# Kernel tuning notes

Hardware: AMD Instinct MI355X
Metric: run time of the kernel (lower is better)

Reference implementation:

```python
import jax, jax.numpy as jnp
import numpy as np

N_HEAD = 16
N_KV_HEAD = 4
N_EMBD = 2048

def rotate_half(x):
    x1, x2 = jnp.split(x, 2, axis=-1)
    return jnp.concatenate([-x2, x1], axis=-1)

def rope_tables(T, k):
    # angles = 10000^(-2*i/k) for i in [0, k/2); cos/sin repeated twice along last dim
    inv = jnp.power(10000.0, -2.0 * jnp.arange(k // 2, dtype=jnp.float32) / k)
    ang = jnp.arange(T, dtype=jnp.float32)[:, None] * inv[None, :]  # [T, k/2]
    cos = jnp.tile(jnp.cos(ang), (1, 2))  # [T, k]
    sin = jnp.tile(jnp.sin(ang), (1, 2))
    return cos, sin

def setup_inputs() -> dict:
    key = jax.random.key(0)
    ks = jax.random.split(key, 5)
    B, T, D = 4, 1024, N_EMBD
    g, h = N_KV_HEAD, N_HEAD
    k = D // h
    s = 0.02
    return {
        'x': jax.random.normal(ks[0], (B, T, D), dtype=jnp.float32),
        'Wq': jax.random.normal(ks[1], (D, D), dtype=jnp.float32) * s,
        'Wk': jax.random.normal(ks[2], (D, g * k), dtype=jnp.float32) * s,
        'Wv': jax.random.normal(ks[3], (D, g * k), dtype=jnp.float32) * s,
        'Wo': jax.random.normal(ks[4], (D, D), dtype=jnp.float32) * s,
    }

def reference(x, Wq, Wk, Wv, Wo):
    B, T, D = x.shape
    h, g = N_HEAD, N_KV_HEAD
    k = D // h
    Q = (x @ Wq).reshape(B, T, h, k).transpose(0, 2, 1, 3)  # [B,h,T,k]
    K = (x @ Wk).reshape(B, T, g, k).transpose(0, 2, 1, 3)  # [B,g,T,k]
    V = (x @ Wv).reshape(B, T, g, k).transpose(0, 2, 1, 3)
    # GQA: repeat_interleave kv heads to match query heads
    K = jnp.repeat(K, h // g, axis=1)  # [B,h,T,k]
    V = jnp.repeat(V, h // g, axis=1)
    cos, sin = rope_tables(T, k)
    cos = cos[None, None]  # [1,1,T,k]
    sin = sin[None, None]
    Q = Q * cos + rotate_half(Q) * sin
    K = K * cos + rotate_half(K) * sin
    scores = jnp.einsum('bhqk,bhsk->bhqs', Q, K) / jnp.sqrt(jnp.float32(k))
    causal = jnp.tril(jnp.ones((T, T), dtype=bool))
    scores = jnp.where(causal[None, None], scores, -jnp.inf)
    A = jax.nn.softmax(scores, axis=-1)
    Y = jnp.einsum('bhqs,bhsk->bhqk', A, V)
    Y = Y.transpose(0, 2, 1, 3).reshape(B, T, D)
    return Y @ Wo
```

## Files before the change

### kernel.cpp

```cpp
#include <hip/hip_runtime.h>
#include <math.h>

#define B_ 4
#define T_ 1024
#define D_ 2048
#define NH 16
#define NKV 4
#define HD 128
#define KV_D 512
#define QKV_S 2560

typedef __attribute__((ext_vector_type(8))) short short8;
typedef __attribute__((ext_vector_type(4))) float f32x4;

__device__ __forceinline__ ushort f2b(float f) {
    unsigned u = __float_as_uint(f);
    return (ushort)((u + 0x7fffu + ((u >> 16) & 1u)) >> 16);
}
__device__ __forceinline__ float b2f(ushort u) {
    return __uint_as_float((unsigned)u << 16);
}

#if __has_builtin(__builtin_amdgcn_exp2f)
#define EXP2F(x) __builtin_amdgcn_exp2f(x)
#else
#define EXP2F(x) __expf((x) * 0.6931471805599453f)
#endif

#define ASYNC_COPY16(g, l)                                                  \
    __builtin_amdgcn_global_load_lds(                                       \
        (const __attribute__((address_space(1))) void*)(g),                 \
        (__attribute__((address_space(3))) void*)(l), 16, 0, 0)

__global__ __launch_bounds__(256) void prep_all(const float* __restrict__ x,
                                                const float* __restrict__ Wq,
                                                const float* __restrict__ Wk,
                                                const float* __restrict__ Wv,
                                                const float* __restrict__ Wo,
                                                ushort* __restrict__ xb,
                                                ushort* __restrict__ WqkvT,
                                                ushort* __restrict__ WoT,
                                                float2* __restrict__ tab) {
    __shared__ float tile[32][33];
    const int bid = blockIdx.x;
    if (bid < 8192) {
        const int i = bid * 256 + threadIdx.x;
        const float4 v = ((const float4*)x)[i];
        ushort4 u;
        u.x = f2b(v.x); u.y = f2b(v.y); u.z = f2b(v.z); u.w = f2b(v.w);
        ((ushort4*)xb)[i] = u;
        return;
    }
    if (bid >= 18432) {
        const int idx = (bid - 18432) * 256 + threadIdx.x;
        const int t = idx >> 6, i = idx & 63;
        const float inv = exp2f((float)i * (-13.287712379549449f / 64.0f));
        const float ang = (float)t * inv;
        tab[idx] = make_float2(cosf(ang), sinf(ang));
        return;
    }
    const float* W;
    ushort* WT;
    int N, rb;
    if (bid < 12288)      { W = Wq; WT = WqkvT;                           N = D_;   rb = bid - 8192; }
    else if (bid < 13312) { W = Wk; WT = WqkvT + (size_t)D_ * D_;         N = KV_D; rb = bid - 12288; }
    else if (bid < 14336) { W = Wv; WT = WqkvT + (size_t)(D_+KV_D) * D_;  N = KV_D; rb = bid - 13312; }
    else                  { W = Wo; WT = WoT;                             N = D_;   rb = bid - 14336; }
    const int bxn = N / 32;
    const int n0 = (rb % bxn) * 32, k0 = (rb / bxn) * 32;
    const int tx = threadIdx.x & 31, ty = threadIdx.x >> 5;
    for (int i = ty; i < 32; i += 8)
        tile[i][tx] = W[(size_t)(k0 + i) * N + n0 + tx];
    __syncthreads();
    for (int i = ty; i < 32; i += 8)
        WT[(size_t)(n0 + i) * D_ + k0 + tx] = f2b(tile[tx][i]);
}

__global__ __launch_bounds__(256) void gemm_qkv(const ushort* __restrict__ A,
                                                const ushort* __restrict__ BT,
                                                ushort* __restrict__ QKV,
                                                ushort* __restrict__ Vt,
                                                const float2* __restrict__ tab) {
    __shared__ ushort smem[128 * 136];
    ushort* As = smem;
    ushort* Bs = smem + 4096;
    const int K = D_;
    const int tid = threadIdx.x;
    const int m0 = blockIdx.y * 128, n0 = blockIdx.x * 128;
    const int hid = n0 >> 7;
    const int wave = tid >> 6, lane = tid & 63;
    const int wm = (wave >> 1) * 64, wn = (wave & 1) * 64;
    const int lrow = lane & 15;
    const int quad = lane >> 4;

    f32x4 acc[4][4];
    const f32x4 zero = {0.f, 0.f, 0.f, 0.f};
#pragma unroll
    for (int i = 0; i < 4; ++i)
#pragma unroll
        for (int j = 0; j < 4; ++j) acc[i][j] = zero;

    const int srow = tid >> 2;
    const int scol = (tid & 3) * 8;
    const ushort* Ag = A + (size_t)(m0 + srow) * K + scol;
    const ushort* Bg = BT + (size_t)(n0 + srow) * K + scol;
    ushort* AsT = As + tid * 8;
    ushort* BsT = Bs + tid * 8;

    for (int k0 = 0; k0 < K; k0 += 32) {
        ASYNC_COPY16(Ag + k0, AsT);
        ASYNC_COPY16(Ag + k0 + (size_t)64 * K, AsT + 64 * 32);
        ASYNC_COPY16(Bg + k0, BsT);
        ASYNC_COPY16(Bg + k0 + (size_t)64 * K, BsT + 64 * 32);
        __syncthreads();

        short8 a[4], b[4];
#pragma unroll
        for (int mt = 0; mt < 4; ++mt)
            a[mt] = *(const short8*)&As[(wm + mt * 16 + lrow) * 32 + quad * 8];
#pragma unroll
        for (int nt = 0; nt < 4; ++nt)
            b[nt] = *(const short8*)&Bs[(wn + nt * 16 + lrow) * 32 + quad * 8];
#pragma unroll
        for (int mt = 0; mt < 4; ++mt)
#pragma unroll
            for (int nt = 0; nt < 4; ++nt)
                acc[mt][nt] = __builtin_amdgcn_mfma_f32_16x16x32_bf16(
                    a[mt], b[nt], acc[mt][nt], 0, 0, 0);
        __syncthreads();
    }

    ushort* Epi = smem;
#pragma unroll
    for (int mt = 0; mt < 4; ++mt)
#pragma unroll
        for (int nt = 0; nt < 4; ++nt)
#pragma unroll
            for (int r = 0; r < 4; ++r)
                Epi[(wm + mt * 16 + quad * 4 + r) * 136 + wn + nt * 16 + lrow] =
                    f2b(acc[mt][nt][r]);
    __syncthreads();

    const int b = m0 >> 10;
    const int t0 = m0 & 1023;

    if (hid < NH + NKV) {
        const bool isQ = hid < NH;
        const size_t colbase = isQ ? hid * HD : (size_t)D_ + (hid - NH) * HD;
        const float sc = isQ ? (0.08838834764831845f * 1.4426950408889634f) : 1.0f;
        const int r = tid >> 1;
        const int hf = tid & 1;
        const int t = t0 + r;
        ushort* orow = QKV + (size_t)(m0 + r) * QKV_S + colbase;
        const float4* tab4 = (const float4*)tab;
#pragma unroll
        for (int jj = 0; jj < 4; ++jj) {
            const int dbase = hf * 32 + jj * 8;
            const short8 lo = *(const short8*)&Epi[r * 136 + dbase];
            const short8 hi = *(const short8*)&Epi[r * 136 + 64 + dbase];
            ushort olo[8], ohi[8];
#pragma unroll
            for (int k = 0; k < 4; ++k) {
                const float4 cs = tab4[((t * 64 + dbase) >> 1) + k];
                const float x1a = b2f(lo[2 * k]),     x2a = b2f(hi[2 * k]);
                const float x1b = b2f(lo[2 * k + 1]), x2b = b2f(hi[2 * k + 1]);
                olo[2 * k]     = f2b((x1a * cs.x - x2a * cs.y) * sc);
                ohi[2 * k]     = f2b((x2a * cs.x + x1a * cs.y) * sc);
                olo[2 * k + 1] = f2b((x1b * cs.z - x2b * cs.w) * sc);
                ohi[2 * k + 1] = f2b((x2b * cs.z + x1b * cs.w) * sc);
            }
            *(short8*)&orow[dbase]      = *(short8*)olo;
            *(short8*)&orow[dbase + 64] = *(short8*)ohi;
        }
    } else {
        const int kv = hid - (NH + NKV);
        const int d = tid & 127;
        const int hf = tid >> 7;
        ushort* vrow = Vt + ((size_t)((b * NKV + kv) * HD + d)) * T_ + t0 + hf * 64;
#pragma unroll
        for (int jj = 0; jj < 8; ++jj) {
            ushort pk[8];
#pragma unroll
            for (int k = 0; k < 8; ++k)
                pk[k] = Epi[(hf * 64 + jj * 8 + k) * 136 + d];
            *(short8*)&vrow[jj * 8] = *(short8*)pk;
        }
    }
}

__global__ __launch_bounds__(256) void gemm_bf16(const ushort* __restrict__ A,
                                                 const ushort* __restrict__ BT,
                                                 float* __restrict__ C,
                                                 int M, int N, int K) {
    __shared__ ushort As[128 * 32];
    __shared__ ushort Bs[128 * 32];
    const int tid = threadIdx.x;
    const int m0 = blockIdx.y * 128, n0 = blockIdx.x * 128;
    const int wave = tid >> 6, lane = tid & 63;
    const int wm = (wave >> 1) * 64, wn = (wave & 1) * 64;
    const int lrow = lane & 15;
    const int quad = lane >> 4;

    f32x4 acc[4][4];
    const f32x4 zero = {0.f, 0.f, 0.f, 0.f};
#pragma unroll
    for (int i = 0; i < 4; ++i)
#pragma unroll
        for (int j = 0; j < 4; ++j) acc[i][j] = zero;

    const int srow = tid >> 2;
    const int scol = (tid & 3) * 8;
    const ushort* Ag = A + (size_t)(m0 + srow) * K + scol;
    const ushort* Bg = BT + (size_t)(n0 + srow) * K + scol;
    ushort* AsT = As + tid * 8;
    ushort* BsT = Bs + tid * 8;

    for (int k0 = 0; k0 < K; k0 += 32) {
        ASYNC_COPY16(Ag + k0, AsT);
        ASYNC_COPY16(Ag + k0 + (size_t)64 * K, AsT + 64 * 32);
        ASYNC_COPY16(Bg + k0, BsT);
        ASYNC_COPY16(Bg + k0 + (size_t)64 * K, BsT + 64 * 32);
        __syncthreads();

        short8 a[4], b[4];
#pragma unroll
        for (int mt = 0; mt < 4; ++mt)
            a[mt] = *(const short8*)&As[(wm + mt * 16 + lrow) * 32 + quad * 8];
#pragma unroll
        for (int nt = 0; nt < 4; ++nt)
            b[nt] = *(const short8*)&Bs[(wn + nt * 16 + lrow) * 32 + quad * 8];
#pragma unroll
        for (int mt = 0; mt < 4; ++mt)
#pragma unroll
            for (int nt = 0; nt < 4; ++nt)
                acc[mt][nt] = __builtin_amdgcn_mfma_f32_16x16x32_bf16(
                    a[mt], b[nt], acc[mt][nt], 0, 0, 0);
        __syncthreads();
    }

    const int crow = quad * 4;
    const int ccol = lrow;
#pragma unroll
    for (int mt = 0; mt < 4; ++mt)
#pragma unroll
        for (int nt = 0; nt < 4; ++nt)
#pragma unroll
            for (int r = 0; r < 4; ++r)
                C[(size_t)(m0 + wm + mt * 16 + crow + r) * N +
                  n0 + wn + nt * 16 + ccol] = acc[mt][nt][r];
}

__global__ __launch_bounds__(256) void attn_mfma(const ushort* __restrict__ QKV,
                                                 const ushort* __restrict__ Vt,
                                                 ushort* __restrict__ Yb) {
    __shared__ ushort Ks[64][136];
    __shared__ ushort Vs[128][72];
    __shared__ ushort Ps[4][16][72];

    const int bh = blockIdx.x;
    const int qt = (int)gridDim.y - 1 - (int)blockIdx.y;
    const int b = bh >> 4, h = bh & 15;
    const int kvh = h >> 2;
    const int q0 = qt * 64;
    const int tid = threadIdx.x;
    const int wave = tid >> 6, lane = tid & 63;
    const int ln = lane & 15, quad = lane >> 4;

    short8 qf[4];
    {
        const ushort* qp = QKV + ((size_t)(b * T_ + q0 + wave * 16 + ln)) * QKV_S + h * HD + quad * 8;
#pragma unroll
        for (int f = 0; f < 4; ++f) qf[f] = *(const short8*)(qp + f * 32);
    }

    f32x4 acc[8];
    const f32x4 zero = {0.f, 0.f, 0.f, 0.f};
#pragma unroll
    for (int j = 0; j < 8; ++j) acc[j] = zero;
    float m_r[4], l_r[4];
#pragma unroll
    for (int r = 0; r < 4; ++r) { m_r[r] = -INFINITY; l_r[r] = 0.f; }

    const int qrow = q0 + wave * 16 + quad * 4;

    for (int kt = 0; kt <= qt; ++kt) {
        const int s0 = kt * 64;
        __syncthreads();
#pragma unroll
        for (int c = 0; c < 4; ++c) {
            const int cid = tid + 256 * c;
            const int s = cid >> 4, ch = cid & 15;
            *(short8*)&Ks[s][ch * 8] =
                *(const short8*)&QKV[((size_t)(b * T_ + s0 + s)) * QKV_S + D_ + kvh * HD + ch * 8];
        }
#pragma unroll
        for (int c = 0; c < 4; ++c) {
            const int cid = tid + 256 * c;
            const int d = cid >> 3, ch = cid & 7;
            *(short8*)&Vs[d][ch * 8] =
                *(const short8*)&Vt[((size_t)((b * NKV + kvh) * HD + d)) * T_ + s0 + ch * 8];
        }
        __syncthreads();

        float sc[4][4];
#pragma unroll
        for (int ct = 0; ct < 4; ++ct) {
            f32x4 s4 = zero;
#pragma unroll
            for (int f = 0; f < 4; ++f)
                s4 = __builtin_amdgcn_mfma_f32_16x16x32_bf16(
                    qf[f], *(const short8*)&Ks[ct * 16 + ln][f * 32 + quad * 8], s4, 0, 0, 0);
#pragma unroll
            for (int r = 0; r < 4; ++r) sc[ct][r] = s4[r];
        }
        if (kt == qt) {
#pragma unroll
            for (int ct = 0; ct < 4; ++ct)
#pragma unroll
                for (int r = 0; r < 4; ++r)
                    if (s0 + ct * 16 + ln > qrow + r) sc[ct][r] = -INFINITY;
        }
        float alpha[4];
#pragma unroll
        for (int r = 0; r < 4; ++r) {
            float mx = fmaxf(fmaxf(sc[0][r], sc[1][r]), fmaxf(sc[2][r], sc[3][r]));
            mx = fmaxf(mx, __shfl_xor(mx, 1));
            mx = fmaxf(mx, __shfl_xor(mx, 2));
            mx = fmaxf(mx, __shfl_xor(mx, 4));
            mx = fmaxf(mx, __shfl_xor(mx, 8));
            const float mnew = fmaxf(m_r[r], mx);
            alpha[r] = EXP2F(m_r[r] - mnew);
            m_r[r] = mnew;
#pragma unroll
            for (int ct = 0; ct < 4; ++ct) sc[ct][r] = EXP2F(sc[ct][r] - mnew);
            float sum = (sc[0][r] + sc[1][r]) + (sc[2][r] + sc[3][r]);
            sum += __shfl_xor(sum, 1);
            sum += __shfl_xor(sum, 2);
            sum += __shfl_xor(sum, 4);
            sum += __shfl_xor(sum, 8);
            l_r[r] = l_r[r] * alpha[r] + sum;
        }
#pragma unroll
        for (int ct = 0; ct < 4; ++ct)
#pragma unroll
            for (int r = 0; r < 4; ++r)
                Ps[wave][quad * 4 + r][ct * 16 + ln] = f2b(sc[ct][r]);
#pragma unroll
        for (int j = 0; j < 8; ++j)
#pragma unroll
            for (int r = 0; r < 4; ++r) acc[j][r] *= alpha[r];
        const short8 pa0 = *(const short8*)&Ps[wave][ln][quad * 8];
        const short8 pa1 = *(const short8*)&Ps[wave][ln][32 + quad * 8];
#pragma unroll
        for (int j = 0; j < 8; ++j) {
            acc[j] = __builtin_amdgcn_mfma_f32_16x16x32_bf16(
                pa0, *(const short8*)&Vs[j * 16 + ln][quad * 8], acc[j], 0, 0, 0);
            acc[j] = __builtin_amdgcn_mfma_f32_16x16x32_bf16(
                pa1, *(const short8*)&Vs[j * 16 + ln][32 + quad * 8], acc[j], 0, 0, 0);
        }
    }

    float invl[4];
#pragma unroll
    for (int r = 0; r < 4; ++r) invl[r] = 1.f / l_r[r];
    ushort* yb = Yb + ((size_t)(b * T_ + qrow)) * D_ + h * HD + ln;
#pragma unroll
    for (int r = 0; r < 4; ++r)
#pragma unroll
        for (int j = 0; j < 8; ++j)
            yb[(size_t)r * D_ + j * 16] = f2b(acc[j][r] * invl[r]);
}

extern "C" void kernel_launch(void* const* d_in, const int* in_sizes, int n_in,
                              void* d_out, int out_size, void* d_ws, size_t ws_size,
                              hipStream_t stream) {
    const float* x  = (const float*)d_in[0];
    const float* Wq = (const float*)d_in[1];
    const float* Wk = (const float*)d_in[2];
    const float* Wv = (const float*)d_in[3];
    const float* Wo = (const float*)d_in[4];
    float* out = (float*)d_out;

    char* w = (char*)d_ws;
    ushort* xb    = (ushort*)w;  w += (size_t)4096 * D_ * 2;
    ushort* WqkvT = (ushort*)w;  w += (size_t)3072 * D_ * 2;
    ushort* QKV   = (ushort*)w;  w += (size_t)4096 * QKV_S * 2;
    ushort* Vt    = (ushort*)w;  w += (size_t)B_ * KV_D * T_ * 2;
    ushort* Yb    = (ushort*)w;  w += (size_t)4096 * D_ * 2;
    ushort* WoT   = (ushort*)w;  w += (size_t)D_ * D_ * 2;
    float2* tab   = (float2*)w;  w += (size_t)T_ * 64 * 8;

    const int M = B_ * T_;
    dim3 blk(256);

    prep_all<<<18688, blk, 0, stream>>>(x, Wq, Wk, Wv, Wo, xb, WqkvT, WoT, tab);

    gemm_qkv<<<dim3(3072 / 128, M / 128), blk, 0, stream>>>(xb, WqkvT, QKV, Vt, tab);

    attn_mfma<<<dim3(B_ * NH, T_ / 64), blk, 0, stream>>>(QKV, Vt, Yb);

    gemm_bf16<<<dim3(D_ / 128, M / 128), blk, 0, stream>>>(Yb, WoT, out, M, D_, D_);
}
```

Before: 298.3 us.

## Replace QKV GEMM with 256x256 double-buffered, swizzled, phase-scheduled MFMA kernel

The fused QKV projection GEMM moves from 128x128 tiles with 256 threads to 256x256 tiles with 512 threads. It uses 128 KB of dynamic LDS, double-buffers the K=64 slices, and XOR-swizzles the LDS layout. The main loop is split into four MFMA phases with explicit barriers, waitcnts, sched_barriers and setprio, so global-to-LDS copies for the next slice overlap with math. The RoPE/V-transpose epilogue is done in two 128-column halves. The larger tile raises data reuse and hides load latency, but the grid drops to 192 blocks, which may leave some CUs idle.

```diff
diff --git a/kernel.cpp b/kernel.cpp
--- a/kernel.cpp
+++ b/kernel.cpp
@@ -31,6 +31,22 @@
     __builtin_amdgcn_global_load_lds(                                       \
         (const __attribute__((address_space(1))) void*)(g),                 \
         (__attribute__((address_space(3))) void*)(l), 16, 0, 0)
+
+#define SBAR()                                                              \
+    do {                                                                    \
+        __builtin_amdgcn_sched_barrier(0);                                  \
+        asm volatile("" ::: "memory");                                      \
+        __builtin_amdgcn_s_barrier();                                       \
+        asm volatile("" ::: "memory");                                      \
+        __builtin_amdgcn_sched_barrier(0);                                  \
+    } while (0)
+#define WAITV(n) asm volatile("s_waitcnt vmcnt(" #n ")" ::: "memory")
+#define LGKM0()                                                             \
+    do {                                                                    \
+        asm volatile("s_waitcnt lgkmcnt(0)" ::: "memory");                  \
+        __builtin_amdgcn_sched_barrier(0);                                  \
+    } while (0)
+#define MFMA16(ap, bp, cc) cc = __builtin_amdgcn_mfma_f32_16x16x32_bf16(ap, bp, cc, 0, 0, 0)
 
 __global__ __launch_bounds__(256) void prep_all(const float* __restrict__ x,
                                                 const float* __restrict__ Wq,
@@ -76,115 +92,219 @@
         WT[(size_t)(n0 + i) * D_ + k0 + tx] = f2b(tile[tx][i]);
 }
 
-__global__ __launch_bounds__(256) void gemm_qkv(const ushort* __restrict__ A,
-                                                const ushort* __restrict__ BT,
-                                                ushort* __restrict__ QKV,
-                                                ushort* __restrict__ Vt,
-                                                const float2* __restrict__ tab) {
-    __shared__ ushort smem[128 * 136];
-    ushort* As = smem;
-    ushort* Bs = smem + 4096;
+__global__ __launch_bounds__(512, 2) void gemm_qkv256(const ushort* __restrict__ A,
+                                                      const ushort* __restrict__ BT,
+                                                      ushort* __restrict__ QKV,
+                                                      ushort* __restrict__ Vt,
+                                                      const float2* __restrict__ tab) {
+    extern __shared__ ushort smem[];
     const int K = D_;
+    const int NT = K / 64;
     const int tid = threadIdx.x;
-    const int m0 = blockIdx.y * 128, n0 = blockIdx.x * 128;
-    const int hid = n0 >> 7;
+    const int m0 = blockIdx.y * 256, n0 = blockIdx.x * 256;
     const int wave = tid >> 6, lane = tid & 63;
-    const int wm = (wave >> 1) * 64, wn = (wave & 1) * 64;
-    const int lrow = lane & 15;
-    const int quad = lane >> 4;
-
-    f32x4 acc[4][4];
+    const int wr = wave >> 2, wc = wave & 3;
+    const int ln = lane & 15, quad = lane >> 4;
+
+    const int rl = tid >> 3;
+    const int cu = (tid & 7) * 8;
+    const int cus = cu ^ ((rl & 1) << 5);
+    const ushort* Ag = A + (size_t)(m0 + rl) * K + cus;
+    const ushort* Bg = BT + (size_t)(n0 + rl) * K + cus;
+    ushort* const Asl = smem;
+    ushort* const stA = Asl + tid * 8;
+    ushort* const stB = smem + 32768 + tid * 8;
+
+    const int kse = (ln & 1) << 5;
+    const int afrag0 = wr * 8192 + ln * 64 + quad * 8;
+    const int bfrag0 = 32768 + (wc >> 1) * 8192 + ((wc & 1) * 64 + ln) * 64 + quad * 8;
+
+    f32x4 acc[8][4];
     const f32x4 zero = {0.f, 0.f, 0.f, 0.f};
 #pragma unroll
-    for (int i = 0; i < 4; ++i)
+    for (int i = 0; i < 8; ++i)
 #pragma unroll
         for (int j = 0; j < 4; ++j) acc[i][j] = zero;
 
-    const int srow = tid >> 2;
-    const int scol = (tid & 3) * 8;
-    const ushort* Ag = A + (size_t)(m0 + srow) * K + scol;
-    const ushort* Bg = BT + (size_t)(n0 + srow) * K + scol;
-    ushort* AsT = As + tid * 8;
-    ushort* BsT = Bs + tid * 8;
-
-    for (int k0 = 0; k0 < K; k0 += 32) {
-        ASYNC_COPY16(Ag + k0, AsT);
-        ASYNC_COPY16(Ag + k0 + (size_t)64 * K, AsT + 64 * 32);
-        ASYNC_COPY16(Bg + k0, BsT);
-        ASYNC_COPY16(Bg + k0 + (size_t)64 * K, BsT + 64 * 32);
-        __syncthreads();
-
-        short8 a[4], b[4];
+#pragma unroll
+    for (int h = 0; h < 2; ++h)
+#pragma unroll
+        for (int i = 0; i < 2; ++i)
+            ASYNC_COPY16(Ag + (size_t)(h * 128 + i * 64) * K, stA + h * 8192 + i * 4096);
+#pragma unroll
+    for (int h = 0; h < 2; ++h)
+#pragma unroll
+        for (int i = 0; i < 2; ++i)
+            ASYNC_COPY16(Bg + (size_t)(h * 128 + i * 64) * K, stB + h * 8192 + i * 4096);
+
+    for (int t = 0; t < NT; ++t) {
+        const int d = t & 1;
+        const int db = d * 16384;
+        const int dn = (d ^ 1) * 16384;
+        const ushort* Agk = Ag + (t + 1) * 64;
+        const ushort* Bgk = Bg + (t + 1) * 64;
+        if (t + 1 < NT) {
+#pragma unroll
+            for (int h = 0; h < 2; ++h)
+#pragma unroll
+                for (int i = 0; i < 2; ++i)
+                    ASYNC_COPY16(Agk + (size_t)(h * 128 + i * 64) * K,
+                                 stA + dn + h * 8192 + i * 4096);
+            WAITV(4);
+        } else {
+            WAITV(0);
+        }
+        SBAR();
+
+        short8 a[4][2], b0[2][2], b1[2][2];
+        const ushort* Ah = Asl + db + afrag0;
+        const ushort* Bh = smem + db + bfrag0;
+
+#pragma unroll
+        for (int mt = 0; mt < 4; ++mt) {
+            a[mt][0] = *(const short8*)(Ah + mt * 1024 + (0 ^ kse));
+            a[mt][1] = *(const short8*)(Ah + mt * 1024 + (32 ^ kse));
+        }
+#pragma unroll
+        for (int nt = 0; nt < 2; ++nt) {
+            b0[nt][0] = *(const short8*)(Bh + nt * 1024 + (0 ^ kse));
+            b0[nt][1] = *(const short8*)(Bh + nt * 1024 + (32 ^ kse));
+        }
+        if (t + 1 < NT) {
+            ASYNC_COPY16(Bgk, stB + dn);
+            ASYNC_COPY16(Bgk + (size_t)64 * K, stB + dn + 4096);
+        }
+        SBAR();
+        LGKM0();
+        __builtin_amdgcn_s_setprio(1);
 #pragma unroll
         for (int mt = 0; mt < 4; ++mt)
-            a[mt] = *(const short8*)&As[(wm + mt * 16 + lrow) * 32 + quad * 8];
-#pragma unroll
-        for (int nt = 0; nt < 4; ++nt)
-            b[nt] = *(const short8*)&Bs[(wn + nt * 16 + lrow) * 32 + quad * 8];
+#pragma unroll
+            for (int nt = 0; nt < 2; ++nt) {
+                MFMA16(a[mt][0], b0[nt][0], acc[mt][nt]);
+                MFMA16(a[mt][1], b0[nt][1], acc[mt][nt]);
+            }
+        __builtin_amdgcn_s_setprio(0);
+        SBAR();
+
+#pragma unroll
+        for (int nt = 0; nt < 2; ++nt) {
+            b1[nt][0] = *(const short8*)(Bh + 2048 + nt * 1024 + (0 ^ kse));
+            b1[nt][1] = *(const short8*)(Bh + 2048 + nt * 1024 + (32 ^ kse));
+        }
+        if (t + 1 < NT) {
+            ASYNC_COPY16(Bgk + (size_t)128 * K, stB + dn + 8192);
+            ASYNC_COPY16(Bgk + (size_t)192 * K, stB + dn + 12288);
+        }
+        SBAR();
+        LGKM0();
+        __builtin_amdgcn_s_setprio(1);
 #pragma unroll
         for (int mt = 0; mt < 4; ++mt)
 #pragma unroll
-            for (int nt = 0; nt < 4; ++nt)
-                acc[mt][nt] = __builtin_amdgcn_mfma_f32_16x16x32_bf16(
-                    a[mt], b[nt], acc[mt][nt], 0, 0, 0);
-        __syncthreads();
-    }
-
+            for (int nt = 0; nt < 2; ++nt) {
+                MFMA16(a[mt][0], b1[nt][0], acc[mt][2 + nt]);
+                MFMA16(a[mt][1], b1[nt][1], acc[mt][2 + nt]);
+            }
+        __builtin_amdgcn_s_setprio(0);
+        SBAR();
+
+#pragma unroll
+        for (int mt = 0; mt < 4; ++mt) {
+            a[mt][0] = *(const short8*)(Ah + 4096 + mt * 1024 + (0 ^ kse));
+            a[mt][1] = *(const short8*)(Ah + 4096 + mt * 1024 + (32 ^ kse));
+        }
+        SBAR();
+        LGKM0();
+        __builtin_amdgcn_s_setprio(1);
+#pragma unroll
+        for (int mt = 0; mt < 4; ++mt)
+#pragma unroll
+            for (int nt = 0; nt < 2; ++nt) {
+                MFMA16(a[mt][0], b1[nt][0], acc[4 + mt][2 + nt]);
+                MFMA16(a[mt][1], b1[nt][1], acc[4 + mt][2 + nt]);
+            }
+        __builtin_amdgcn_s_setprio(0);
+        SBAR();
+
+        SBAR();
+        LGKM0();
+        __builtin_amdgcn_s_setprio(1);
+#pragma unroll
+        for (int mt = 0; mt < 4; ++mt)
+#pragma unroll
+            for (int nt = 0; nt < 2; ++nt) {
+                MFMA16(a[mt][0], b0[nt][0], acc[4 + mt][nt]);
+                MFMA16(a[mt][1], b0[nt][1], acc[4 + mt][nt]);
+            }
+        __builtin_amdgcn_s_setprio(0);
+        SBAR();
+    }
+
+    __syncthreads();
     ushort* Epi = smem;
-#pragma unroll
-    for (int mt = 0; mt < 4; ++mt)
-#pragma unroll
-        for (int nt = 0; nt < 4; ++nt)
-#pragma unroll
-            for (int r = 0; r < 4; ++r)
-                Epi[(wm + mt * 16 + quad * 4 + r) * 136 + wn + nt * 16 + lrow] =
-                    f2b(acc[mt][nt][r]);
-    __syncthreads();
-
     const int b = m0 >> 10;
     const int t0 = m0 & 1023;
-
-    if (hid < NH + NKV) {
-        const bool isQ = hid < NH;
-        const size_t colbase = isQ ? hid * HD : (size_t)D_ + (hid - NH) * HD;
-        const float sc = isQ ? (0.08838834764831845f * 1.4426950408889634f) : 1.0f;
-        const int r = tid >> 1;
-        const int hf = tid & 1;
-        const int t = t0 + r;
-        ushort* orow = QKV + (size_t)(m0 + r) * QKV_S + colbase;
-        const float4* tab4 = (const float4*)tab;
-#pragma unroll
-        for (int jj = 0; jj < 4; ++jj) {
-            const int dbase = hf * 32 + jj * 8;
-            const short8 lo = *(const short8*)&Epi[r * 136 + dbase];
-            const short8 hi = *(const short8*)&Epi[r * 136 + 64 + dbase];
-            ushort olo[8], ohi[8];
-#pragma unroll
-            for (int k = 0; k < 4; ++k) {
-                const float4 cs = tab4[((t * 64 + dbase) >> 1) + k];
-                const float x1a = b2f(lo[2 * k]),     x2a = b2f(hi[2 * k]);
-                const float x1b = b2f(lo[2 * k + 1]), x2b = b2f(hi[2 * k + 1]);
-                olo[2 * k]     = f2b((x1a * cs.x - x2a * cs.y) * sc);
-                ohi[2 * k]     = f2b((x2a * cs.x + x1a * cs.y) * sc);
-                olo[2 * k + 1] = f2b((x1b * cs.z - x2b * cs.w) * sc);
-                ohi[2 * k + 1] = f2b((x2b * cs.z + x1b * cs.w) * sc);
+    const int hid0 = n0 >> 7;
+
+    for (int hh = 0; hh < 2; ++hh) {
+        if ((wc >> 1) == hh) {
+            const int cb = (wc & 1) * 64;
+#pragma unroll
+            for (int am = 0; am < 8; ++am)
+#pragma unroll
+                for (int an = 0; an < 4; ++an)
+#pragma unroll
+                    for (int r = 0; r < 4; ++r)
+                        Epi[(wr * 128 + am * 16 + quad * 4 + r) * 136 + cb + an * 16 + ln] =
+                            f2b(acc[am][an][r]);
+        }
+        __syncthreads();
+
+        const int hid = hid0 + hh;
+        if (hid < NH + NKV) {
+            const bool isQ = hid < NH;
+            const size_t colbase = isQ ? (size_t)hid * HD : (size_t)D_ + (size_t)(hid - NH) * HD;
+            const float sc = isQ ? (0.08838834764831845f * 1.4426950408889634f) : 1.0f;
+            const int r = tid >> 1;
+            const int hf = tid & 1;
+            const int tt = t0 + r;
+            ushort* orow = QKV + (size_t)(m0 + r) * QKV_S + colbase;
+            const float4* tab4 = (const float4*)tab;
+#pragma unroll
+            for (int jj = 0; jj < 4; ++jj) {
+                const int dbase = hf * 32 + jj * 8;
+                const short8 lo = *(const short8*)&Epi[r * 136 + dbase];
+                const short8 hi = *(const short8*)&Epi[r * 136 + 64 + dbase];
+                ushort olo[8], ohi[8];
+#pragma unroll
+                for (int kq = 0; kq < 4; ++kq) {
+                    const float4 cs = tab4[((tt * 64 + dbase) >> 1) + kq];
+                    const float x1a = b2f(lo[2 * kq]),     x2a = b2f(hi[2 * kq]);
+                    const float x1b = b2f(lo[2 * kq + 1]), x2b = b2f(hi[2 * kq + 1]);
+                    olo[2 * kq]     = f2b((x1a * cs.x - x2a * cs.y) * sc);
+                    ohi[2 * kq]     = f2b((x2a * cs.x + x1a * cs.y) * sc);
+                    olo[2 * kq + 1] = f2b((x1b * cs.z - x2b * cs.w) * sc);
+                    ohi[2 * kq + 1] = f2b((x2b * cs.z + x1b * cs.w) * sc);
+                }
+                *(short8*)&orow[dbase]      = *(short8*)olo;
+                *(short8*)&orow[dbase + 64] = *(short8*)ohi;
             }
-            *(short8*)&orow[dbase]      = *(short8*)olo;
-            *(short8*)&orow[dbase + 64] = *(short8*)ohi;
-        }
-    } else {
-        const int kv = hid - (NH + NKV);
-        const int d = tid & 127;
-        const int hf = tid >> 7;
-        ushort* vrow = Vt + ((size_t)((b * NKV + kv) * HD + d)) * T_ + t0 + hf * 64;
-#pragma unroll
-        for (int jj = 0; jj < 8; ++jj) {
-            ushort pk[8];
-#pragma unroll
-            for (int k = 0; k < 8; ++k)
-                pk[k] = Epi[(hf * 64 + jj * 8 + k) * 136 + d];
-            *(short8*)&vrow[jj * 8] = *(short8*)pk;
-        }
+        } else {
+            const int kv = hid - (NH + NKV);
+            const int dd = tid & 127;
+            const int th = tid >> 7;
+            ushort* vrow = Vt + ((size_t)((b * NKV + kv) * HD + dd)) * T_ + t0 + th * 64;
+#pragma unroll
+            for (int jj = 0; jj < 8; ++jj) {
+                ushort pk[8];
+#pragma unroll
+                for (int k2 = 0; k2 < 8; ++k2)
+                    pk[k2] = Epi[(th * 64 + jj * 8 + k2) * 136 + dd];
+                *(short8*)&vrow[jj * 8] = *(short8*)pk;
+            }
+        }
+        __syncthreads();
     }
 }
 
@@ -393,9 +513,12 @@
     const int M = B_ * T_;
     dim3 blk(256);
 
+    hipFuncSetAttribute(reinterpret_cast<const void*>(gemm_qkv256),
+                        hipFuncAttributeMaxDynamicSharedMemorySize, 131072);
+
     prep_all<<<18688, blk, 0, stream>>>(x, Wq, Wk, Wv, Wo, xb, WqkvT, WoT, tab);
 
-    gemm_qkv<<<dim3(3072 / 128, M / 128), blk, 0, stream>>>(xb, WqkvT, QKV, Vt, tab);
+    gemm_qkv256<<<dim3(3072 / 256, M / 256), dim3(512), 131072, stream>>>(xb, WqkvT, QKV, Vt, tab);
 
     attn_mfma<<<dim3(B_ * NH, T_ / 64), blk, 0, stream>>>(QKV, Vt, Yb);
 
```

After: 321.3 us. 1.08x slower.
